# Kernel tuning notes

Measured on AMD Instinct MI355X. Metric: run time of the kernel, lower is better.

Reference implementation:

```python
import jax, jax.numpy as jnp
import numpy as np

BATCH = 131072
HASHLEN = 64
HID = 180
OUT = 300


def setup_inputs() -> dict:
    key = jax.random.key(0)
    ks = jax.random.split(key, 8)
    scale = 0.05
    return {
        "b": jax.random.normal(ks[0], (BATCH, HASHLEN), dtype=jnp.float32),
        "labels": jax.random.randint(ks[1], (BATCH,), 0, 300),
        "W_h": jax.random.normal(ks[2], (HID, HASHLEN), dtype=jnp.float32) * scale,
        "b_h": jax.random.normal(ks[3], (HID,), dtype=jnp.float32) * scale,
        "W_mu": jax.random.normal(ks[4], (OUT, HID), dtype=jnp.float32) * scale,
        "b_mu": jax.random.normal(ks[5], (OUT,), dtype=jnp.float32) * scale,
        "W_sig": jax.random.normal(ks[6], (OUT, HID), dtype=jnp.float32) * scale,
        "b_sig": jax.random.normal(ks[7], (OUT,), dtype=jnp.float32) * scale,
    }


def reference(b, labels, W_h, b_h, W_mu, b_mu, W_sig, b_sig):
    # h = hidden(b); mean = mu(h); sigma = sigma_layer(h)
    h = b @ W_h.T + b_h                      # [B, 180]
    mean = h @ W_mu.T + b_mu                 # [B, 300]
    sig = h @ W_sig.T + b_sig                # [B, 300]
    # Original builds diag(sig^2) and calls MVN.rsample, which Cholesky-factors
    # the diagonal covariance: L = diag(sqrt(sig^2)) = diag(|sig|).
    # rsample = mean + L @ eps  ==  mean + |sig| * eps  (elementwise).
    std = jnp.abs(sig)
    eps = jax.random.normal(jax.random.key(42), mean.shape, dtype=mean.dtype)
    return mean + std * eps
```

## Files before the change

### kernel.cpp

```cpp
#include <hip/hip_runtime.h>
#include <stdint.h>

#define BATCH   131072
#define HASHLEN 64
#define HID     180
#define OUT     300

#define BM      64
#define NT      256
#define NTILE2  19

#define WH_FRAGS  (12 * 2 * 64)
#define WM_FRAGS  (NTILE2 * 6 * 64)
#define TOT_FRAGS (WH_FRAGS + 2 * WM_FRAGS)
#define WS_NEEDED ((size_t)TOT_FRAGS * 16)

typedef short bf16x8 __attribute__((ext_vector_type(8)));
typedef float f32x4  __attribute__((ext_vector_type(4)));

#define FAST_SQRT(x) __builtin_amdgcn_sqrtf(x)
#define ROTL(x, r) __builtin_amdgcn_alignbit((x), (x), 32u - (r))

__device__ __forceinline__ unsigned threefry_bits(unsigned ctr) {
  const unsigned ks0 = 0u;
  const unsigned ks1 = 42u;
  const unsigned ks2 = 0x1BD11BDAu ^ 0u ^ 42u;
  unsigned x0 = ks0;
  unsigned x1 = ctr + ks1;
#define TF_R(r) { x0 += x1; x1 = ROTL(x1, r); x1 ^= x0; }
  TF_R(13u) TF_R(15u) TF_R(26u) TF_R(6u)
  x0 += ks1; x1 += ks2 + 1u;
  TF_R(17u) TF_R(29u) TF_R(16u) TF_R(24u)
  x0 += ks2; x1 += ks0 + 2u;
  TF_R(13u) TF_R(15u) TF_R(26u) TF_R(6u)
  x0 += ks0; x1 += ks1 + 3u;
  TF_R(17u) TF_R(29u) TF_R(16u) TF_R(24u)
  x0 += ks1; x1 += ks2 + 4u;
  TF_R(13u) TF_R(15u) TF_R(26u) TF_R(6u)
  x0 += ks2; x1 += ks0 + 5u;
#undef TF_R
  return x0 ^ x1;
}

__device__ __forceinline__ float poly_low_sqrt2(float zz) {
  float p = 2.11772e-09f;
  p = fmaf(p, zz, 3.73196e-08f);
  p = fmaf(p, zz, -5.52613e-07f);
  p = fmaf(p, zz, -9.93702e-07f);
  p = fmaf(p, zz, 7.13551e-05f);
  p = fmaf(p, zz, -5.90464e-04f);
  p = fmaf(p, zz, -2.83858e-03f);
  p = fmaf(p, zz, 0.24177160f);
  p = fmaf(p, zz, 2.1233136f);
  return p;
}
__device__ __forceinline__ float poly_high_sqrt2(float v) {
  float p = -6.53600e-05f;
  p = fmaf(p, v, 3.95852e-05f);
  p = fmaf(p, v, 6.35506e-04f);
  p = fmaf(p, v, -2.07827e-03f);
  p = fmaf(p, v, 3.89984e-03f);
  p = fmaf(p, v, -6.22117e-03f);
  p = fmaf(p, v, 9.25254e-03f);
  p = fmaf(p, v, 1.1793807f);
  p = fmaf(p, v, 4.0064340f);
  return p;
}

__device__ __forceinline__ uint16_t f2bf(float f) {
  uint32_t u = __float_as_uint(f);
  return (uint16_t)((u + 0x7FFFu + ((u >> 16) & 1u)) >> 16);
}

__global__ __launch_bounds__(256) void prep_weights(
    const float* __restrict__ W_h, const float* __restrict__ W_mu,
    const float* __restrict__ W_sig, uint16_t* __restrict__ ws)
{
  int f = blockIdx.x * 256 + threadIdx.x;
  if (f >= TOT_FRAGS) return;
  uint16_t vals[8];
  if (f < WH_FRAGS) {
    int nt = f >> 7, s = (f >> 6) & 1, l = f & 63;
    int row = nt * 16 + (l & 15);
    int k0  = s * 32 + (l >> 4) * 8;
#pragma unroll
    for (int j = 0; j < 8; ++j)
      vals[j] = (row < HID) ? f2bf(W_h[row * HASHLEN + k0 + j]) : (uint16_t)0;
  } else {
    int g = f - WH_FRAGS;
    const float* W = (g < WM_FRAGS) ? W_mu : W_sig;
    if (g >= WM_FRAGS) g -= WM_FRAGS;
    int gt = g / 384, s = (g >> 6) % 6, l = g & 63;
    int col = gt * 16 + (l & 15);
    int k0  = s * 32 + (l >> 4) * 8;
#pragma unroll
    for (int j = 0; j < 8; ++j) {
      int k = k0 + j;
      vals[j] = (col < OUT && k < HID) ? f2bf(W[col * HID + k]) : (uint16_t)0;
    }
  }
  uint16_t* dst = ws + (size_t)f * 8;
#pragma unroll
  for (int j = 0; j < 8; ++j) dst[j] = vals[j];
}

__device__ __forceinline__ void epilogue4(
    f32x4 accM, f32x4 accS, f32x4 bm4, f32x4 bs4, uint32_t gi0,
    float* __restrict__ out)
{
  uint32_t bits[4];
#pragma unroll
  for (int q = 0; q < 4; ++q)
    bits[q] = threefry_bits(gi0 + (uint32_t)q);
  float xx[4], z[4], pl[4];
#pragma unroll
  for (int q = 0; q < 4; ++q) {
    float f = __uint_as_float((bits[q] >> 9) | 0x3F800000u) - 1.0f;
    const float LO = -0.99999994f;
    float u = fmaxf(LO, fmaf(f, 2.0f, LO));
    xx[q] = u;
    float t = fmaf(-u, u, 1.0f);
    z[q] = -__log2f(t);
    pl[q] = poly_low_sqrt2(z[q] - 3.6067376f);
  }
#pragma unroll
  for (int q = 0; q < 4; ++q) {
    if (__any(z[q] >= 7.2134752f)) {
      float v = FAST_SQRT(z[q]) - 3.6033669f;
      float ph = poly_high_sqrt2(v);
      pl[q] = (z[q] >= 7.2134752f) ? ph : pl[q];
    }
  }
  f32x4 res;
#pragma unroll
  for (int q = 0; q < 4; ++q) {
    float mu  = accM[q] + bm4[q];
    float sg  = fabsf(accS[q] + bs4[q]);
    res[q] = fmaf(sg, pl[q] * xx[q], mu);
  }
  *(f32x4*)(out + gi0) = res;
}

__global__ __launch_bounds__(NT, 6) void fused_decoder(
    const float* __restrict__ bin,
    const uint16_t* __restrict__ ws,
    const float* __restrict__ b_h,
    const float* __restrict__ b_mu, const float* __restrict__ b_sig,
    float* __restrict__ out)
{
  __shared__ unsigned char lds[BM * 384];

  const int tid    = threadIdx.x;
  const int l      = tid & 63;
  const int w      = tid >> 6;
  const int lane15 = l & 15;
  const int lhi    = l >> 4;
  const int swzb   = (lane15 & 7) << 4;
  const int row0   = blockIdx.x * BM;
  const int r0     = w * 16;

  const bf16x8* wsWh = (const bf16x8*)ws;
  const bf16x8* wsWm = (const bf16x8*)ws + WH_FRAGS;
  const bf16x8* wsWs = (const bf16x8*)ws + WH_FRAGS + WM_FRAGS;

  {
    const float* brow = bin + (size_t)(row0 + r0 + lane15) * HASHLEN;
    bf16x8 bfrag[2];
#pragma unroll
    for (int s = 0; s < 2; ++s) {
      float4 v0 = *(const float4*)(brow + s * 32 + lhi * 8);
      float4 v1 = *(const float4*)(brow + s * 32 + lhi * 8 + 4);
      bf16x8 a;
      a[0] = (short)f2bf(v0.x); a[1] = (short)f2bf(v0.y);
      a[2] = (short)f2bf(v0.z); a[3] = (short)f2bf(v0.w);
      a[4] = (short)f2bf(v1.x); a[5] = (short)f2bf(v1.y);
      a[6] = (short)f2bf(v1.z); a[7] = (short)f2bf(v1.w);
      bfrag[s] = a;
    }
    const int row = r0 + lane15;
#pragma unroll
    for (int nt = 0; nt < 12; ++nt) {
      f32x4 acc = {0.f, 0.f, 0.f, 0.f};
#pragma unroll
      for (int s = 0; s < 2; ++s)
        acc = __builtin_amdgcn_mfma_f32_16x16x32_bf16(wsWh[(nt * 2 + s) * 64 + l], bfrag[s], acc, 0, 0, 0);
      const int k0 = nt * 16 + lhi * 4;
      f32x4 bias = {0.f, 0.f, 0.f, 0.f};
      if (k0 <= HID - 4) bias = *(const f32x4*)(b_h + k0);
      const bool ok = (k0 < HID);
      float h0 = ok ? (acc[0] + bias[0]) : 0.0f;
      float h1 = ok ? (acc[1] + bias[1]) : 0.0f;
      float h2 = ok ? (acc[2] + bias[2]) : 0.0f;
      float h3 = ok ? (acc[3] + bias[3]) : 0.0f;
      uint2 pk;
      pk.x = (uint32_t)f2bf(h0) | ((uint32_t)f2bf(h1) << 16);
      pk.y = (uint32_t)f2bf(h2) | ((uint32_t)f2bf(h3) << 16);
      *(uint2*)(lds + row * 384 + ((2 * k0) ^ swzb)) = pk;
    }
  }

  bf16x8 a2[6];
#pragma unroll
  for (int s = 0; s < 6; ++s)
    a2[s] = *(const bf16x8*)(lds + (r0 + lane15) * 384 + ((s * 64 + lhi * 16) ^ swzb));

  const uint32_t idx0 = (uint32_t)((row0 + r0 + lane15) * OUT + lhi * 4);

#pragma unroll 1
  for (int gt = 0; gt < NTILE2 - 1; ++gt) {
    f32x4 accM = {0.f, 0.f, 0.f, 0.f};
    f32x4 accS = {0.f, 0.f, 0.f, 0.f};
#pragma unroll
    for (int s = 0; s < 6; ++s)
      accM = __builtin_amdgcn_mfma_f32_16x16x32_bf16(wsWm[(gt * 6 + s) * 64 + l], a2[s], accM, 0, 0, 0);
#pragma unroll
    for (int s = 0; s < 6; ++s)
      accS = __builtin_amdgcn_mfma_f32_16x16x32_bf16(wsWs[(gt * 6 + s) * 64 + l], a2[s], accS, 0, 0, 0);
    const int c0 = gt * 16 + lhi * 4;
    f32x4 bm4 = *(const f32x4*)(b_mu + c0);
    f32x4 bs4 = *(const f32x4*)(b_sig + c0);
    epilogue4(accM, accS, bm4, bs4, idx0 + (uint32_t)(gt * 16), out);
  }

  {
    const int gt = NTILE2 - 1;
    f32x4 accM = {0.f, 0.f, 0.f, 0.f};
    f32x4 accS = {0.f, 0.f, 0.f, 0.f};
#pragma unroll
    for (int s = 0; s < 6; ++s) {
      accM = __builtin_amdgcn_mfma_f32_16x16x32_bf16(wsWm[(gt * 6 + s) * 64 + l], a2[s], accM, 0, 0, 0);
      accS = __builtin_amdgcn_mfma_f32_16x16x32_bf16(wsWs[(gt * 6 + s) * 64 + l], a2[s], accS, 0, 0, 0);
    }
    if (lhi < 3) {
      const int c0 = gt * 16 + lhi * 4;
      f32x4 bm4 = *(const f32x4*)(b_mu + c0);
      f32x4 bs4 = *(const f32x4*)(b_sig + c0);
      epilogue4(accM, accS, bm4, bs4, idx0 + (uint32_t)(gt * 16), out);
    }
  }
}

#define FTILE2  19
#define FCHT    2
#define FNCH    10
#define FSH_OFF   0
#define FSH_BYTES (64 * 384)
#define FU_OFF    FSH_BYTES
#define FSB_OFF   FU_OFF
#define FSWH_OFF  (FU_OFF + 8192)
#define FSWM_OFF  FU_OFF
#define FSWS_OFF  (FU_OFF + 12288)
#define FLDS_BYTES (FSH_BYTES + 32768)

__device__ __forceinline__ float eps_from_bits(uint32_t bits) {
  float f = __uint_as_float((bits >> 9) | 0x3F800000u) - 1.0f;
  const float LO = -0.99999994f;
  float u = fmaxf(LO, fmaf(f, 2.0f, LO));
  float t = fmaf(-u, u, 1.0f);
  float z = -__log2f(t);
  float p = poly_low_sqrt2(z - 3.6067376f);
  if (__any(z >= 7.2134752f)) {
    float ph = poly_high_sqrt2(FAST_SQRT(z) - 3.6033669f);
    p = (z >= 7.2134752f) ? ph : p;
  }
  return p * u;
}

__global__ __launch_bounds__(NT) void fused_decoder_fb(
    const float* __restrict__ bin,
    const float* __restrict__ W_h, const float* __restrict__ b_h,
    const float* __restrict__ W_mu, const float* __restrict__ b_mu,
    const float* __restrict__ W_sig, const float* __restrict__ b_sig,
    float* __restrict__ out)
{
  __shared__ unsigned char lds[FLDS_BYTES];
  const int tid = threadIdx.x;
  const int l = tid & 63, w = tid >> 6;
  const int lane15 = l & 15, lhi = l >> 4;
  const int swzb = (l & 7) << 4;
  const int row0 = blockIdx.x * BM;
  const int r0 = w * 16;
  {
    const float4* src = reinterpret_cast<const float4*>(bin + (size_t)row0 * HASHLEN);
#pragma unroll
    for (int it = 0; it < 4; ++it) {
      int idx = tid + NT * it;
      int r = idx >> 4, k4 = idx & 15;
      float4 v = src[idx];
      uint32_t p0 = f2bf(v.x) | ((uint32_t)f2bf(v.y) << 16);
      uint32_t p1 = f2bf(v.z) | ((uint32_t)f2bf(v.w) << 16);
      int off = FSB_OFF + r * 128 + ((k4 * 8) ^ ((r & 7) << 4));
      *(uint32_t*)(lds + off) = p0;
      *(uint32_t*)(lds + off + 4) = p1;
    }
#pragma unroll
    for (int it = 0; it < 12; ++it) {
      int idx = tid + NT * it;
      int n = idx >> 4, k4 = idx & 15;
      float4 v = make_float4(0.f, 0.f, 0.f, 0.f);
      if (n < HID) v = *(const float4*)(W_h + (size_t)n * HASHLEN + k4 * 4);
      uint32_t p0 = f2bf(v.x) | ((uint32_t)f2bf(v.y) << 16);
      uint32_t p1 = f2bf(v.z) | ((uint32_t)f2bf(v.w) << 16);
      int off = FSWH_OFF + n * 128 + ((k4 * 8) ^ ((n & 7) << 4));
      *(uint32_t*)(lds + off) = p0;
      *(uint32_t*)(lds + off + 4) = p1;
    }
  }
  __syncthreads();
  {
    bf16x8 a1[2];
#pragma unroll
    for (int s = 0; s < 2; ++s)
      a1[s] = *(const bf16x8*)(lds + FSB_OFF + (r0 + lane15) * 128 + ((s * 64 + lhi * 16) ^ swzb));
#pragma unroll
    for (int nt = 0; nt < 12; ++nt) {
      f32x4 acc = {0.f, 0.f, 0.f, 0.f};
#pragma unroll
      for (int s = 0; s < 2; ++s) {
        bf16x8 bf = *(const bf16x8*)(lds + FSWH_OFF + (nt * 16 + lane15) * 128 + ((s * 64 + lhi * 16) ^ swzb));
        acc = __builtin_amdgcn_mfma_f32_16x16x32_bf16(a1[s], bf, acc, 0, 0, 0);
      }
      int col = nt * 16 + lane15;
      float bias = (col < HID) ? b_h[col] : 0.0f;
#pragma unroll
      for (int q = 0; q < 4; ++q) {
        int row = r0 + lhi * 4 + q;
        float h = (col < HID) ? (acc[q] + bias) : 0.0f;
        *(uint16_t*)(lds + FSH_OFF + row * 384 + ((2 * col) ^ ((row & 7) << 4))) = f2bf(h);
      }
    }
  }
  __syncthreads();
  bf16x8 a2[6];
#pragma unroll
  for (int s = 0; s < 6; ++s)
    a2[s] = *(const bf16x8*)(lds + FSH_OFF + (r0 + lane15) * 384 + ((s * 64 + lhi * 16) ^ swzb));
  const int rowi = tid >> 3;
  const int tt8 = tid & 7;
  for (int ch = 0; ch < FNCH; ++ch) {
    const int t0 = ch * FCHT;
    const int ntc = (FTILE2 - t0 < FCHT) ? (FTILE2 - t0) : FCHT;
    if (rowi < ntc * 16) {
      int col = ch * 32 + rowi;
      bool cok = (col < OUT);
      const float* wm = W_mu + (size_t)col * HID;
      const float* wsg = W_sig + (size_t)col * HID;
#pragma unroll
      for (int it = 0; it < 12; ++it) {
        int k2 = tt8 + 8 * it;
        bool kok = cok && (k2 < 90);
        float2 vm = kok ? *(const float2*)(wm + k2 * 2) : make_float2(0.f, 0.f);
        float2 vs = kok ? *(const float2*)(wsg + k2 * 2) : make_float2(0.f, 0.f);
        int off = (k2 * 4) ^ ((rowi & 7) << 4);
        *(uint32_t*)(lds + FSWM_OFF + rowi * 384 + off) = f2bf(vm.x) | ((uint32_t)f2bf(vm.y) << 16);
        *(uint32_t*)(lds + FSWS_OFF + rowi * 384 + off) = f2bf(vs.x) | ((uint32_t)f2bf(vs.y) << 16);
      }
    }
    __syncthreads();
    for (int nt2 = 0; nt2 < ntc; ++nt2) {
      const int gt = t0 + nt2;
      const int crow = nt2 * 16 + lane15;
      f32x4 accM = {0.f, 0.f, 0.f, 0.f};
      f32x4 accS = {0.f, 0.f, 0.f, 0.f};
#pragma unroll
      for (int s = 0; s < 6; ++s) {
        int boff = (s * 64 + lhi * 16) ^ swzb;
        bf16x8 bm = *(const bf16x8*)(lds + FSWM_OFF + crow * 384 + boff);
        bf16x8 bs = *(const bf16x8*)(lds + FSWS_OFF + crow * 384 + boff);
        accM = __builtin_amdgcn_mfma_f32_16x16x32_bf16(a2[s], bm, accM, 0, 0, 0);
        accS = __builtin_amdgcn_mfma_f32_16x16x32_bf16(a2[s], bs, accS, 0, 0, 0);
      }
      const int col = gt * 16 + lane15;
      if (col < OUT) {
        const float bmu = b_mu[col];
        const float bsg = b_sig[col];
#pragma unroll
        for (int q = 0; q < 4; ++q) {
          int row = r0 + lhi * 4 + q;
          int gr = row0 + row;
          float mu = accM[q] + bmu;
          float sg = fabsf(accS[q] + bsg);
          uint32_t gi = (uint32_t)(gr * OUT + col);
          uint32_t bits = threefry_bits(gi);
          float eps = eps_from_bits(bits);
          out[(size_t)gr * OUT + col] = fmaf(sg, eps, mu);
        }
      }
    }
    __syncthreads();
  }
}

extern "C" void kernel_launch(void* const* d_in, const int* in_sizes, int n_in,
                              void* d_out, int out_size, void* d_ws, size_t ws_size,
                              hipStream_t stream) {
  const float* b     = (const float*)d_in[0];
  const float* W_h   = (const float*)d_in[2];
  const float* b_h   = (const float*)d_in[3];
  const float* W_mu  = (const float*)d_in[4];
  const float* b_mu  = (const float*)d_in[5];
  const float* W_sig = (const float*)d_in[6];
  const float* b_sig = (const float*)d_in[7];
  float* out = (float*)d_out;

  if (ws_size >= WS_NEEDED && d_ws != nullptr) {
    uint16_t* ws = (uint16_t*)d_ws;
    hipLaunchKernelGGL(prep_weights, dim3((TOT_FRAGS + 255) / 256), dim3(256), 0, stream,
                       W_h, W_mu, W_sig, ws);
    hipLaunchKernelGGL(fused_decoder, dim3(BATCH / BM), dim3(NT), 0, stream,
                       b, ws, b_h, b_mu, b_sig, out);
  } else {
    hipLaunchKernelGGL(fused_decoder_fb, dim3(BATCH / BM), dim3(NT), 0, stream,
                       b, W_h, b_h, W_mu, b_mu, W_sig, b_sig, out);
  }
}
```

Before: 145.3 us.

## Precompute Gaussian noise into bf16 workspace buffer in a separate kernel

Adds a gen_eps kernel that evaluates the threefry RNG and inverse-erf normal transform for all BATCH*OUT elements and stores them as bf16 in the workspace. The main decoder then loads the precomputed noise instead of generating it inline, moving ALU-heavy work out of the MFMA kernel. This adds a 78 MB write and a 78 MB read of memory traffic plus an extra launch, and rounding eps to bf16 loses precision relative to the reference. The path runs only when the workspace is large enough; otherwise the old kernel is used.

```diff
diff --git a/kernel.cpp b/kernel.cpp
--- a/kernel.cpp
+++ b/kernel.cpp
@@ -14,6 +14,10 @@
 #define WM_FRAGS  (NTILE2 * 6 * 64)
 #define TOT_FRAGS (WH_FRAGS + 2 * WM_FRAGS)
 #define WS_NEEDED ((size_t)TOT_FRAGS * 16)
+
+#define EPS_OFF   WS_NEEDED
+#define EPS_ELEMS ((size_t)BATCH * OUT)
+#define WS_FULL   (EPS_OFF + EPS_ELEMS * 2)
 
 typedef short bf16x8 __attribute__((ext_vector_type(8)));
 typedef float f32x4  __attribute__((ext_vector_type(4)));
@@ -67,6 +71,20 @@
   return p;
 }
 
+__device__ __forceinline__ float eps_from_bits(uint32_t bits) {
+  float f = __uint_as_float((bits >> 9) | 0x3F800000u) - 1.0f;
+  const float LO = -0.99999994f;
+  float u = fmaxf(LO, fmaf(f, 2.0f, LO));
+  float t = fmaf(-u, u, 1.0f);
+  float z = -__log2f(t);
+  float p = poly_low_sqrt2(z - 3.6067376f);
+  if (__any(z >= 7.2134752f)) {
+    float ph = poly_high_sqrt2(FAST_SQRT(z) - 3.6033669f);
+    p = (z >= 7.2134752f) ? ph : p;
+  }
+  return p * u;
+}
+
 __device__ __forceinline__ uint16_t f2bf(float f) {
   uint32_t u = __float_as_uint(f);
   return (uint16_t)((u + 0x7FFFu + ((u >> 16) & 1u)) >> 16);
@@ -104,46 +122,65 @@
   for (int j = 0; j < 8; ++j) dst[j] = vals[j];
 }
 
-__device__ __forceinline__ void epilogue4(
-    f32x4 accM, f32x4 accS, f32x4 bm4, f32x4 bs4, uint32_t gi0,
-    float* __restrict__ out)
-{
-  uint32_t bits[4];
-#pragma unroll
-  for (int q = 0; q < 4; ++q)
-    bits[q] = threefry_bits(gi0 + (uint32_t)q);
-  float xx[4], z[4], pl[4];
-#pragma unroll
-  for (int q = 0; q < 4; ++q) {
-    float f = __uint_as_float((bits[q] >> 9) | 0x3F800000u) - 1.0f;
+__global__ __launch_bounds__(256) void gen_eps(uint16_t* __restrict__ eps)
+{
+  const uint32_t t    = blockIdx.x * 256 + threadIdx.x;
+  const uint32_t base = t * 8u;
+  uint32_t bits[8];
+#pragma unroll
+  for (int j = 0; j < 8; ++j) bits[j] = threefry_bits(base + (uint32_t)j);
+  float e[8], z[8], pl[8], xx[8];
+#pragma unroll
+  for (int j = 0; j < 8; ++j) {
+    float f = __uint_as_float((bits[j] >> 9) | 0x3F800000u) - 1.0f;
     const float LO = -0.99999994f;
     float u = fmaxf(LO, fmaf(f, 2.0f, LO));
-    xx[q] = u;
-    float t = fmaf(-u, u, 1.0f);
-    z[q] = -__log2f(t);
-    pl[q] = poly_low_sqrt2(z[q] - 3.6067376f);
-  }
+    xx[j] = u;
+    float tq = fmaf(-u, u, 1.0f);
+    z[j] = -__log2f(tq);
+    pl[j] = poly_low_sqrt2(z[j] - 3.6067376f);
+  }
+#pragma unroll
+  for (int j = 0; j < 8; ++j) {
+    if (__any(z[j] >= 7.2134752f)) {
+      float ph = poly_high_sqrt2(FAST_SQRT(z[j]) - 3.6033669f);
+      pl[j] = (z[j] >= 7.2134752f) ? ph : pl[j];
+    }
+    e[j] = pl[j] * xx[j];
+  }
+  uint32_t pk[4];
+#pragma unroll
+  for (int j = 0; j < 4; ++j) {
+    uint32_t r;
+    asm("v_cvt_pk_bf16_f32 %0, %1, %2" : "=v"(r) : "v"(e[2 * j]), "v"(e[2 * j + 1]));
+    pk[j] = r;
+  }
+  *(uint4*)(eps + base) = make_uint4(pk[0], pk[1], pk[2], pk[3]);
+}
+
+__device__ __forceinline__ void epilogue4_eps(
+    f32x4 accM, f32x4 accS, f32x4 bm4, f32x4 bs4, uint2 e2, uint32_t gi0,
+    float* __restrict__ out)
+{
+  float ev[4];
+  ev[0] = __uint_as_float(e2.x << 16);
+  ev[1] = __uint_as_float(e2.x & 0xFFFF0000u);
+  ev[2] = __uint_as_float(e2.y << 16);
+  ev[3] = __uint_as_float(e2.y & 0xFFFF0000u);
+  f32x4 res;
 #pragma unroll
   for (int q = 0; q < 4; ++q) {
-    if (__any(z[q] >= 7.2134752f)) {
-      float v = FAST_SQRT(z[q]) - 3.6033669f;
-      float ph = poly_high_sqrt2(v);
-      pl[q] = (z[q] >= 7.2134752f) ? ph : pl[q];
-    }
-  }
-  f32x4 res;
-#pragma unroll
-  for (int q = 0; q < 4; ++q) {
-    float mu  = accM[q] + bm4[q];
-    float sg  = fabsf(accS[q] + bs4[q]);
-    res[q] = fmaf(sg, pl[q] * xx[q], mu);
+    float mu = accM[q] + bm4[q];
+    float sg = accS[q] + bs4[q];
+    res[q] = fmaf(fabsf(sg), ev[q], mu);
   }
   *(f32x4*)(out + gi0) = res;
 }
 
-__global__ __launch_bounds__(NT, 6) void fused_decoder(
+__global__ __launch_bounds__(NT, 6) void fused_decoder_eps(
     const float* __restrict__ bin,
     const uint16_t* __restrict__ ws,
+    const uint16_t* __restrict__ epsb,
     const float* __restrict__ b_h,
     const float* __restrict__ b_mu, const float* __restrict__ b_sig,
     float* __restrict__ out)
@@ -208,6 +245,144 @@
 
 #pragma unroll 1
   for (int gt = 0; gt < NTILE2 - 1; ++gt) {
+    const uint32_t gi0 = idx0 + (uint32_t)(gt * 16);
+    uint2 e2 = *(const uint2*)(epsb + gi0);
+    const int c0 = gt * 16 + lhi * 4;
+    f32x4 bm4 = *(const f32x4*)(b_mu + c0);
+    f32x4 bs4 = *(const f32x4*)(b_sig + c0);
+    f32x4 accM = {0.f, 0.f, 0.f, 0.f};
+    f32x4 accS = {0.f, 0.f, 0.f, 0.f};
+#pragma unroll
+    for (int s = 0; s < 6; ++s)
+      accM = __builtin_amdgcn_mfma_f32_16x16x32_bf16(wsWm[(gt * 6 + s) * 64 + l], a2[s], accM, 0, 0, 0);
+#pragma unroll
+    for (int s = 0; s < 6; ++s)
+      accS = __builtin_amdgcn_mfma_f32_16x16x32_bf16(wsWs[(gt * 6 + s) * 64 + l], a2[s], accS, 0, 0, 0);
+    epilogue4_eps(accM, accS, bm4, bs4, e2, gi0, out);
+  }
+
+  {
+    const int gt = NTILE2 - 1;
+    f32x4 accM = {0.f, 0.f, 0.f, 0.f};
+    f32x4 accS = {0.f, 0.f, 0.f, 0.f};
+#pragma unroll
+    for (int s = 0; s < 6; ++s) {
+      accM = __builtin_amdgcn_mfma_f32_16x16x32_bf16(wsWm[(gt * 6 + s) * 64 + l], a2[s], accM, 0, 0, 0);
+      accS = __builtin_amdgcn_mfma_f32_16x16x32_bf16(wsWs[(gt * 6 + s) * 64 + l], a2[s], accS, 0, 0, 0);
+    }
+    if (lhi < 3) {
+      const uint32_t gi0 = idx0 + (uint32_t)(gt * 16);
+      uint2 e2 = *(const uint2*)(epsb + gi0);
+      const int c0 = gt * 16 + lhi * 4;
+      f32x4 bm4 = *(const f32x4*)(b_mu + c0);
+      f32x4 bs4 = *(const f32x4*)(b_sig + c0);
+      epilogue4_eps(accM, accS, bm4, bs4, e2, gi0, out);
+    }
+  }
+}
+
+__device__ __forceinline__ void epilogue4(
+    f32x4 accM, f32x4 accS, f32x4 bm4, f32x4 bs4, uint32_t gi0,
+    float* __restrict__ out)
+{
+  uint32_t bits[4];
+#pragma unroll
+  for (int q = 0; q < 4; ++q)
+    bits[q] = threefry_bits(gi0 + (uint32_t)q);
+  float xx[4], z[4], pl[4];
+#pragma unroll
+  for (int q = 0; q < 4; ++q) {
+    float f = __uint_as_float((bits[q] >> 9) | 0x3F800000u) - 1.0f;
+    const float LO = -0.99999994f;
+    float u = fmaxf(LO, fmaf(f, 2.0f, LO));
+    xx[q] = u;
+    float t = fmaf(-u, u, 1.0f);
+    z[q] = -__log2f(t);
+    pl[q] = poly_low_sqrt2(z[q] - 3.6067376f);
+  }
+#pragma unroll
+  for (int q = 0; q < 4; ++q) {
+    if (__any(z[q] >= 7.2134752f)) {
+      float v = FAST_SQRT(z[q]) - 3.6033669f;
+      float ph = poly_high_sqrt2(v);
+      pl[q] = (z[q] >= 7.2134752f) ? ph : pl[q];
+    }
+  }
+  f32x4 res;
+#pragma unroll
+  for (int q = 0; q < 4; ++q) {
+    float mu  = accM[q] + bm4[q];
+    float sg  = fabsf(accS[q] + bs4[q]);
+    res[q] = fmaf(sg, pl[q] * xx[q], mu);
+  }
+  *(f32x4*)(out + gi0) = res;
+}
+
+__global__ __launch_bounds__(NT, 6) void fused_decoder_ws(
+    const float* __restrict__ bin,
+    const uint16_t* __restrict__ ws,
+    const float* __restrict__ b_h,
+    const float* __restrict__ b_mu, const float* __restrict__ b_sig,
+    float* __restrict__ out)
+{
+  __shared__ unsigned char lds[BM * 384];
+  const int tid    = threadIdx.x;
+  const int l      = tid & 63;
+  const int w      = tid >> 6;
+  const int lane15 = l & 15;
+  const int lhi    = l >> 4;
+  const int swzb   = (lane15 & 7) << 4;
+  const int row0   = blockIdx.x * BM;
+  const int r0     = w * 16;
+
+  const bf16x8* wsWh = (const bf16x8*)ws;
+  const bf16x8* wsWm = (const bf16x8*)ws + WH_FRAGS;
+  const bf16x8* wsWs = (const bf16x8*)ws + WH_FRAGS + WM_FRAGS;
+
+  {
+    const float* brow = bin + (size_t)(row0 + r0 + lane15) * HASHLEN;
+    bf16x8 bfrag[2];
+#pragma unroll
+    for (int s = 0; s < 2; ++s) {
+      float4 v0 = *(const float4*)(brow + s * 32 + lhi * 8);
+      float4 v1 = *(const float4*)(brow + s * 32 + lhi * 8 + 4);
+      bf16x8 a;
+      a[0] = (short)f2bf(v0.x); a[1] = (short)f2bf(v0.y);
+      a[2] = (short)f2bf(v0.z); a[3] = (short)f2bf(v0.w);
+      a[4] = (short)f2bf(v1.x); a[5] = (short)f2bf(v1.y);
+      a[6] = (short)f2bf(v1.z); a[7] = (short)f2bf(v1.w);
+      bfrag[s] = a;
+    }
+    const int row = r0 + lane15;
+#pragma unroll
+    for (int nt = 0; nt < 12; ++nt) {
+      f32x4 acc = {0.f, 0.f, 0.f, 0.f};
+#pragma unroll
+      for (int s = 0; s < 2; ++s)
+        acc = __builtin_amdgcn_mfma_f32_16x16x32_bf16(wsWh[(nt * 2 + s) * 64 + l], bfrag[s], acc, 0, 0, 0);
+      const int k0 = nt * 16 + lhi * 4;
+      f32x4 bias = {0.f, 0.f, 0.f, 0.f};
+      if (k0 <= HID - 4) bias = *(const f32x4*)(b_h + k0);
+      const bool ok = (k0 < HID);
+      float h0 = ok ? (acc[0] + bias[0]) : 0.0f;
+      float h1 = ok ? (acc[1] + bias[1]) : 0.0f;
+      float h2 = ok ? (acc[2] + bias[2]) : 0.0f;
+      float h3 = ok ? (acc[3] + bias[3]) : 0.0f;
+      uint2 pk;
+      pk.x = (uint32_t)f2bf(h0) | ((uint32_t)f2bf(h1) << 16);
+      pk.y = (uint32_t)f2bf(h2) | ((uint32_t)f2bf(h3) << 16);
+      *(uint2*)(lds + row * 384 + ((2 * k0) ^ swzb)) = pk;
+    }
+  }
+  bf16x8 a2[6];
+#pragma unroll
+  for (int s = 0; s < 6; ++s)
+    a2[s] = *(const bf16x8*)(lds + (r0 + lane15) * 384 + ((s * 64 + lhi * 16) ^ swzb));
+
+  const uint32_t idx0 = (uint32_t)((row0 + r0 + lane15) * OUT + lhi * 4);
+
+#pragma unroll 1
+  for (int gt = 0; gt < NTILE2 - 1; ++gt) {
     f32x4 accM = {0.f, 0.f, 0.f, 0.f};
     f32x4 accS = {0.f, 0.f, 0.f, 0.f};
 #pragma unroll
@@ -221,7 +396,6 @@
     f32x4 bs4 = *(const f32x4*)(b_sig + c0);
     epilogue4(accM, accS, bm4, bs4, idx0 + (uint32_t)(gt * 16), out);
   }
-
   {
     const int gt = NTILE2 - 1;
     f32x4 accM = {0.f, 0.f, 0.f, 0.f};
@@ -251,20 +425,6 @@
 #define FSWM_OFF  FU_OFF
 #define FSWS_OFF  (FU_OFF + 12288)
 #define FLDS_BYTES (FSH_BYTES + 32768)
-
-__device__ __forceinline__ float eps_from_bits(uint32_t bits) {
-  float f = __uint_as_float((bits >> 9) | 0x3F800000u) - 1.0f;
-  const float LO = -0.99999994f;
-  float u = fmaxf(LO, fmaf(f, 2.0f, LO));
-  float t = fmaf(-u, u, 1.0f);
-  float z = -__log2f(t);
-  float p = poly_low_sqrt2(z - 3.6067376f);
-  if (__any(z >= 7.2134752f)) {
-    float ph = poly_high_sqrt2(FAST_SQRT(z) - 3.6033669f);
-    p = (z >= 7.2134752f) ? ph : p;
-  }
-  return p * u;
-}
 
 __global__ __launch_bounds__(NT) void fused_decoder_fb(
     const float* __restrict__ bin,
@@ -403,11 +563,20 @@
   const float* b_sig = (const float*)d_in[7];
   float* out = (float*)d_out;
 
-  if (ws_size >= WS_NEEDED && d_ws != nullptr) {
+  if (ws_size >= WS_FULL && d_ws != nullptr) {
+    uint16_t* ws   = (uint16_t*)d_ws;
+    uint16_t* epsb = (uint16_t*)((unsigned char*)d_ws + EPS_OFF);
+    hipLaunchKernelGGL(prep_weights, dim3((TOT_FRAGS + 255) / 256), dim3(256), 0, stream,
+                       W_h, W_mu, W_sig, ws);
+    hipLaunchKernelGGL(gen_eps, dim3((unsigned)(EPS_ELEMS / 8 / 256)), dim3(256), 0, stream,
+                       epsb);
+    hipLaunchKernelGGL(fused_decoder_eps, dim3(BATCH / BM), dim3(NT), 0, stream,
+                       b, ws, epsb, b_h, b_mu, b_sig, out);
+  } else if (ws_size >= WS_NEEDED && d_ws != nullptr) {
     uint16_t* ws = (uint16_t*)d_ws;
     hipLaunchKernelGGL(prep_weights, dim3((TOT_FRAGS + 255) / 256), dim3(256), 0, stream,
                        W_h, W_mu, W_sig, ws);
-    hipLaunchKernelGGL(fused_decoder, dim3(BATCH / BM), dim3(NT), 0, stream,
+    hipLaunchKernelGGL(fused_decoder_ws, dim3(BATCH / BM), dim3(NT), 0, stream,
                        b, ws, b_h, b_mu, b_sig, out);
   } else {
     hipLaunchKernelGGL(fused_decoder_fb, dim3(BATCH / BM), dim3(NT), 0, stream,
```

New measurement: 212.6 us. 46.3% more time.

## Stage second-layer weight fragments through double-buffered LDS via async global_load_lds

Applied to the files above, without the earlier changes.

The W_mu/W_sig fragments for each output tile are now prefetched into a double-buffered LDS region with global_load_lds, one tile ahead, instead of being read directly from global memory by every wave. This aims to cut redundant global/L2 weight traffic across the four waves and hide load latency behind MFMA work. In exchange it adds about 24KB of LDS per block, a barrier and full vmcnt wait every tile, and lowers the launch-bounds occupancy hint from 6 to 3, which may reduce latency hiding. The tail tile is folded into the main loop.

```diff
diff --git a/kernel.cpp b/kernel.cpp
--- a/kernel.cpp
+++ b/kernel.cpp
@@ -15,11 +15,22 @@
 #define TOT_FRAGS (WH_FRAGS + 2 * WM_FRAGS)
 #define WS_NEEDED ((size_t)TOT_FRAGS * 16)
 
+#define FRAG_CHUNK 6144
+#define H_BYTES    (BM * 384)
+#define DBUF_OFF   H_BYTES
+#define LDS_BYTES  (H_BYTES + 2 * 2 * FRAG_CHUNK)
+
 typedef short bf16x8 __attribute__((ext_vector_type(8)));
 typedef float f32x4  __attribute__((ext_vector_type(4)));
 
 #define FAST_SQRT(x) __builtin_amdgcn_sqrtf(x)
 #define ROTL(x, r) __builtin_amdgcn_alignbit((x), (x), 32u - (r))
+
+__device__ __forceinline__ void gload_lds16(const void* g, void* l) {
+  __builtin_amdgcn_global_load_lds(
+      (const __attribute__((address_space(1))) uint32_t*)(uintptr_t)g,
+      (__attribute__((address_space(3))) uint32_t*)(uintptr_t)l, 16, 0, 0);
+}
 
 __device__ __forceinline__ unsigned threefry_bits(unsigned ctr) {
   const unsigned ks0 = 0u;
@@ -67,6 +78,20 @@
   return p;
 }
 
+__device__ __forceinline__ float eps_from_bits(uint32_t bits) {
+  float f = __uint_as_float((bits >> 9) | 0x3F800000u) - 1.0f;
+  const float LO = -0.99999994f;
+  float u = fmaxf(LO, fmaf(f, 2.0f, LO));
+  float t = fmaf(-u, u, 1.0f);
+  float z = -__log2f(t);
+  float p = poly_low_sqrt2(z - 3.6067376f);
+  if (__any(z >= 7.2134752f)) {
+    float ph = poly_high_sqrt2(FAST_SQRT(z) - 3.6033669f);
+    p = (z >= 7.2134752f) ? ph : p;
+  }
+  return p * u;
+}
+
 __device__ __forceinline__ uint16_t f2bf(float f) {
   uint32_t u = __float_as_uint(f);
   return (uint16_t)((u + 0x7FFFu + ((u >> 16) & 1u)) >> 16);
@@ -141,14 +166,14 @@
   *(f32x4*)(out + gi0) = res;
 }
 
-__global__ __launch_bounds__(NT, 6) void fused_decoder(
+__global__ __launch_bounds__(NT, 3) void fused_decoder_stg(
     const float* __restrict__ bin,
     const uint16_t* __restrict__ ws,
     const float* __restrict__ b_h,
     const float* __restrict__ b_mu, const float* __restrict__ b_sig,
     float* __restrict__ out)
 {
-  __shared__ unsigned char lds[BM * 384];
+  __shared__ unsigned char lds[LDS_BYTES];
 
   const int tid    = threadIdx.x;
   const int l      = tid & 63;
@@ -160,8 +185,20 @@
   const int r0     = w * 16;
 
   const bf16x8* wsWh = (const bf16x8*)ws;
-  const bf16x8* wsWm = (const bf16x8*)ws + WH_FRAGS;
-  const bf16x8* wsWs = (const bf16x8*)ws + WH_FRAGS + WM_FRAGS;
+  const unsigned char* wsMB = (const unsigned char*)ws + (size_t)WH_FRAGS * 16;
+  const unsigned char* wsSB = wsMB + (size_t)WM_FRAGS * 16;
+
+  {
+    unsigned char* dbuf = lds + DBUF_OFF;
+#pragma unroll
+    for (int j = 0; j < 3; ++j) {
+      const int slot0 = j * 256 + w * 64;
+      const unsigned char* src = (slot0 < 384)
+          ? wsMB + (size_t)(slot0 + l) * 16
+          : wsSB + (size_t)(slot0 - 384 + l) * 16;
+      gload_lds16(src, dbuf + slot0 * 16);
+    }
+  }
 
   {
     const float* brow = bin + (size_t)(row0 + r0 + lane15) * HASHLEN;
@@ -198,45 +235,59 @@
       *(uint2*)(lds + row * 384 + ((2 * k0) ^ swzb)) = pk;
     }
   }
-
   bf16x8 a2[6];
 #pragma unroll
   for (int s = 0; s < 6; ++s)
     a2[s] = *(const bf16x8*)(lds + (r0 + lane15) * 384 + ((s * 64 + lhi * 16) ^ swzb));
 
+  asm volatile("s_waitcnt vmcnt(0)" ::: "memory");
+  __syncthreads();
+
   const uint32_t idx0 = (uint32_t)((row0 + r0 + lane15) * OUT + lhi * 4);
 
 #pragma unroll 1
-  for (int gt = 0; gt < NTILE2 - 1; ++gt) {
+  for (int gt = 0; gt < NTILE2; ++gt) {
+    if (gt + 1 < NTILE2) {
+      unsigned char* nbuf = lds + DBUF_OFF + ((gt + 1) & 1) * (2 * FRAG_CHUNK);
+      const size_t coff = (size_t)(gt + 1) * FRAG_CHUNK;
+#pragma unroll
+      for (int j = 0; j < 3; ++j) {
+        const int slot0 = j * 256 + w * 64;
+        const unsigned char* src = (slot0 < 384)
+            ? wsMB + coff + (size_t)(slot0 + l) * 16
+            : wsSB + coff + (size_t)(slot0 - 384 + l) * 16;
+        gload_lds16(src, nbuf + slot0 * 16);
+      }
+    }
+
+    const unsigned char* cur = lds + DBUF_OFF + (gt & 1) * (2 * FRAG_CHUNK);
+    bf16x8 fm[6], fs[6];
+#pragma unroll
+    for (int s = 0; s < 6; ++s)
+      fm[s] = *(const bf16x8*)(cur + s * 1024 + l * 16);
+#pragma unroll
+    for (int s = 0; s < 6; ++s)
+      fs[s] = *(const bf16x8*)(cur + FRAG_CHUNK + s * 1024 + l * 16);
+
     f32x4 accM = {0.f, 0.f, 0.f, 0.f};
     f32x4 accS = {0.f, 0.f, 0.f, 0.f};
 #pragma unroll
     for (int s = 0; s < 6; ++s)
-      accM = __builtin_amdgcn_mfma_f32_16x16x32_bf16(wsWm[(gt * 6 + s) * 64 + l], a2[s], accM, 0, 0, 0);
+      accM = __builtin_amdgcn_mfma_f32_16x16x32_bf16(fm[s], a2[s], accM, 0, 0, 0);
 #pragma unroll
     for (int s = 0; s < 6; ++s)
-      accS = __builtin_amdgcn_mfma_f32_16x16x32_bf16(wsWs[(gt * 6 + s) * 64 + l], a2[s], accS, 0, 0, 0);
-    const int c0 = gt * 16 + lhi * 4;
-    f32x4 bm4 = *(const f32x4*)(b_mu + c0);
-    f32x4 bs4 = *(const f32x4*)(b_sig + c0);
-    epilogue4(accM, accS, bm4, bs4, idx0 + (uint32_t)(gt * 16), out);
-  }
-
-  {
-    const int gt = NTILE2 - 1;
-    f32x4 accM = {0.f, 0.f, 0.f, 0.f};
-    f32x4 accS = {0.f, 0.f, 0.f, 0.f};
-#pragma unroll
-    for (int s = 0; s < 6; ++s) {
-      accM = __builtin_amdgcn_mfma_f32_16x16x32_bf16(wsWm[(gt * 6 + s) * 64 + l], a2[s], accM, 0, 0, 0);
-      accS = __builtin_amdgcn_mfma_f32_16x16x32_bf16(wsWs[(gt * 6 + s) * 64 + l], a2[s], accS, 0, 0, 0);
-    }
-    if (lhi < 3) {
+      accS = __builtin_amdgcn_mfma_f32_16x16x32_bf16(fs[s], a2[s], accS, 0, 0, 0);
+
+    const bool tail = (gt == NTILE2 - 1);
+    if (!tail || lhi < 3) {
       const int c0 = gt * 16 + lhi * 4;
       f32x4 bm4 = *(const f32x4*)(b_mu + c0);
       f32x4 bs4 = *(const f32x4*)(b_sig + c0);
       epilogue4(accM, accS, bm4, bs4, idx0 + (uint32_t)(gt * 16), out);
     }
+
+    asm volatile("s_waitcnt vmcnt(0)" ::: "memory");
+    __syncthreads();
   }
 }
 
@@ -251,20 +302,6 @@
 #define FSWM_OFF  FU_OFF
 #define FSWS_OFF  (FU_OFF + 12288)
 #define FLDS_BYTES (FSH_BYTES + 32768)
-
-__device__ __forceinline__ float eps_from_bits(uint32_t bits) {
-  float f = __uint_as_float((bits >> 9) | 0x3F800000u) - 1.0f;
-  const float LO = -0.99999994f;
-  float u = fmaxf(LO, fmaf(f, 2.0f, LO));
-  float t = fmaf(-u, u, 1.0f);
-  float z = -__log2f(t);
-  float p = poly_low_sqrt2(z - 3.6067376f);
-  if (__any(z >= 7.2134752f)) {
-    float ph = poly_high_sqrt2(FAST_SQRT(z) - 3.6033669f);
-    p = (z >= 7.2134752f) ? ph : p;
-  }
-  return p * u;
-}
 
 __global__ __launch_bounds__(NT) void fused_decoder_fb(
     const float* __restrict__ bin,
@@ -407,7 +444,7 @@
     uint16_t* ws = (uint16_t*)d_ws;
     hipLaunchKernelGGL(prep_weights, dim3((TOT_FRAGS + 255) / 256), dim3(256), 0, stream,
                        W_h, W_mu, W_sig, ws);
-    hipLaunchKernelGGL(fused_decoder, dim3(BATCH / BM), dim3(NT), 0, stream,
+    hipLaunchKernelGGL(fused_decoder_stg, dim3(BATCH / BM), dim3(NT), 0, stream,
                        b, ws, b_h, b_mu, b_sig, out);
   } else {
     hipLaunchKernelGGL(fused_decoder_fb, dim3(BATCH / BM), dim3(NT), 0, stream,
```

Measured after the change: 154.3 us. +6.2%, slower.
